# Performance work log

Hardware: AMD Instinct MI355X
Metric: run time of the kernel (lower is better)

The kernel has to match this reference:

```python
import jax, jax.numpy as jnp
import numpy as np

BIG_NEG = -1e9


def setup_inputs() -> dict:
    key = jax.random.key(0)
    ks = jax.random.split(key, 6)
    b, N1, d, C1, K = 4, 511, 64, 31, 32
    features = jax.random.normal(ks[0], (b, N1, d), jnp.float32)
    transition_logits = jax.random.normal(ks[1], (C1, C1), jnp.float32)
    init_logits = jax.random.uniform(ks[2], (C1,), jnp.float32)
    poisson_log_rates = jax.random.normal(ks[3], (C1,), jnp.float32) * 0.5 + 1.5
    A = jax.random.normal(ks[5], (d, d), jnp.float32)
    gaussian_cov = jnp.eye(d, dtype=jnp.float32) + 0.1 * (A @ A.T) / d
    gaussian_means = jax.random.normal(ks[4], (C1, d), jnp.float32) * 0.1
    return {
        "features": features,
        "transition_logits": transition_logits,
        "init_logits": init_logits,
        "poisson_log_rates": poisson_log_rates,
        "gaussian_means": gaussian_means,
        "gaussian_cov": gaussian_cov,
        "max_k": K,
        "add_eos": 1,
    }


def reference(features, transition_logits, init_logits, poisson_log_rates,
              gaussian_means, gaussian_cov, max_k, add_eos):
    b, N1, d = features.shape
    C1 = transition_logits.shape[0]
    K = int(max_k)
    dt = features.dtype

    # transition log-probs: mask diagonal with BIG_NEG, normalize over axis 0 (torch dim=0)
    trans = jax.nn.log_softmax(
        jnp.where(jnp.eye(C1, dtype=bool), jnp.asarray(BIG_NEG, dt), transition_logits), axis=0)
    init = jax.nn.log_softmax(init_logits)

    # Poisson duration log-probs: k*log(rate) - rate - lgamma(k+1), k = 0..K-1
    rates = jnp.exp(poisson_log_rates)  # [C1]
    tsteps = jnp.arange(K, dtype=dt)[:, None]  # [K,1]
    length = tsteps * poisson_log_rates[None, :] - rates[None, :] - jax.scipy.special.gammaln(tsteps + 1.0)  # [K,C1]

    # Gaussian emission log-probs, shared full covariance across classes
    L = jnp.linalg.cholesky(gaussian_cov)
    Linv = jax.scipy.linalg.solve_triangular(L, jnp.eye(d, dtype=dt), lower=True)
    diff = features[:, :, None, :] - gaussian_means[None, None]          # [b,N1,C1,d]
    y = jnp.einsum('bncd,ed->bnce', diff, Linv)
    maha = jnp.sum(y * y, axis=-1)                                       # [b,N1,C1]
    logdet = 2.0 * jnp.sum(jnp.log(jnp.diag(L)))
    emis = -0.5 * (d * jnp.log(jnp.asarray(2.0 * jnp.pi, dt)) + logdet + maha)

    if add_eos:
        N, C = N1 + 1, C1 + 1
        trans_a = jnp.full((C, C), BIG_NEG, dt).at[:C1, :C1].set(trans).at[C1, :].set(0.0)
        init_a = jnp.full((C,), BIG_NEG, dt).at[:C1].set(init)
        length_a = jnp.full((K, C), BIG_NEG, dt).at[:, :C1].set(length).at[1, C1].set(0.0)
        emis_a = jnp.full((b, N, C), BIG_NEG, dt).at[:, :N1, :C1].set(emis).at[:, N1, C1].set(0.0)
    else:
        N, C = N1, C1
        trans_a, init_a, length_a, emis_a = trans, init, length, emis

    ep = jnp.pad(emis_a, ((0, 0), (0, K), (0, 0)))
    cs = jnp.concatenate([jnp.zeros((b, 1, C), dt), jnp.cumsum(ep, axis=1)], axis=1)  # [b,N+K+1,C]
    tt = jnp.arange(N - 1)[:, None]
    kk = jnp.arange(K)[None, :]
    win = cs[:, tt + kk] - cs[:, tt]  # [b, N-1, K, C]

    # edge scores: b x (N-1) x K x C_prev x C
    scores = (trans_a[None, None, None] +
              length_a[None, None, :, None, :] +
              win[:, :, :, None, :])
    scores = scores.at[:, 0].add(init_a[None, None, None, :])
    keos = jnp.arange(1, K)
    scores = scores.at[:, N - 1 - keos, keos].add(emis_a[:, N - 1][:, None, :, None])
    return scores
```

## Files before the change

### kernel.cpp

```cpp
#include <hip/hip_runtime.h>
#include <math.h>

#define BIG_NEG -1.0e9f

typedef float f4 __attribute__((ext_vector_type(4)));

constexpr int B  = 4;
constexpr int N1 = 511;
constexpr int C1 = 31;
constexpr int K  = 32;
constexpr int N  = N1 + 1;
constexpr int C  = C1 + 1;

constexpr int WS_TRANS = 0;
constexpr int WS_INIT  = 1024;
constexpr int WS_LEN   = 1056;
constexpr int WS_P     = 2080;
constexpr int WS_W     = 6176;
constexpr int WS_BIAS  = 8224;
constexpr int WS_EMIS  = 8256;

__global__ __launch_bounds__(512) void k_prep(const float* __restrict__ tl,
                                              const float* __restrict__ il,
                                              const float* __restrict__ plr,
                                              const float* __restrict__ cov,
                                              const float* __restrict__ means,
                                              float* __restrict__ ws) {
    __shared__ float M[64][132];
    __shared__ float cP[2][4][64];
    __shared__ float Bsave[16][16];
    __shared__ float mu[C1][64];

    const int tid = threadIdx.x;
    const int ii = tid >> 3;
    const int cg = tid & 7;

    f4* Mrow = (f4*)&M[ii][0];

    for (int idx = tid; idx < 1024; idx += 512) {
        const int i = idx >> 5, j = idx & 31;
        float lv;
        if (j < C1) {
            float lr = plr[j];
            lv = (float)i * lr - expf(lr) - lgammaf((float)i + 1.0f);
        } else {
            lv = (i == 1) ? 0.0f : BIG_NEG;
        }
        ws[WS_LEN + idx] = lv;
        if (i == C1) ws[WS_TRANS + idx] = 0.0f;
        else if (j == C1) ws[WS_TRANS + idx] = BIG_NEG;
    }
    if (tid < B * C) {
        const int bb = tid >> 5, cc = tid & 31;
        ws[WS_EMIS + (bb * N + N1) * C + cc] = (cc == C1) ? 0.0f : BIG_NEG;
    }
    if (tid < C1) {
        const int jj = tid;
        float m = BIG_NEG;
        for (int r = 0; r < C1; ++r) {
            float v = (r == jj) ? BIG_NEG : tl[r * C1 + jj];
            m = fmaxf(m, v);
        }
        float s = 0.0f;
        for (int r = 0; r < C1; ++r) {
            float v = (r == jj) ? BIG_NEG : tl[r * C1 + jj];
            s += expf(v - m);
        }
        float lse = m + logf(s);
        for (int r = 0; r < C1; ++r) {
            float v = (r == jj) ? BIG_NEG : tl[r * C1 + jj];
            ws[WS_TRANS + r * 32 + jj] = v - lse;
        }
    }
    if (tid == 32) {
        float m = -1.0e30f;
        for (int cc = 0; cc < C1; ++cc) m = fmaxf(m, il[cc]);
        float s = 0.0f;
        for (int cc = 0; cc < C1; ++cc) s += expf(il[cc] - m);
        float lse = m + logf(s);
        for (int cc = 0; cc < C1; ++cc) ws[WS_INIT + cc] = il[cc] - lse;
        ws[WS_INIT + C1] = BIG_NEG;
    }

    {
        Mrow[cg]     = *(const f4*)&cov[ii * 64 + 4 * cg];
        Mrow[cg + 8] = *(const f4*)&cov[ii * 64 + 4 * (cg + 8)];
        const int r0 = 4 * cg, r1 = 4 * (cg + 8);
        f4 e1 = {(ii == r0) ? 1.f : 0.f, (ii == r0 + 1) ? 1.f : 0.f,
                 (ii == r0 + 2) ? 1.f : 0.f, (ii == r0 + 3) ? 1.f : 0.f};
        f4 e2 = {(ii == r1) ? 1.f : 0.f, (ii == r1 + 1) ? 1.f : 0.f,
                 (ii == r1 + 2) ? 1.f : 0.f, (ii == r1 + 3) ? 1.f : 0.f};
        Mrow[cg + 16] = e1;
        Mrow[cg + 24] = e2;
    }
    if (cg == 0) {
        cP[0][0][ii] = cov[ii * 64 + 0];
        cP[0][1][ii] = cov[ii * 64 + 1];
        cP[0][2][ii] = cov[ii * 64 + 2];
        cP[0][3][ii] = cov[ii * 64 + 3];
    }
    for (int idx = tid; idx < C1 * 64; idx += 512)
        mu[idx >> 6][idx & 63] = means[idx];
    __syncthreads();

    float detprod = 1.0f;
    for (int st = 0; st < 16; ++st) {
        const int s = st << 2;
        const int par = st & 1;
        const float T00 = cP[par][0][s + 0], T01 = cP[par][0][s + 1],
                    T02 = cP[par][0][s + 2], T03 = cP[par][0][s + 3];
        const float T10 = cP[par][1][s + 0], T11 = cP[par][1][s + 1],
                    T12 = cP[par][1][s + 2], T13 = cP[par][1][s + 3];
        const float T20 = cP[par][2][s + 0], T21 = cP[par][2][s + 1],
                    T22 = cP[par][2][s + 2], T23 = cP[par][2][s + 3];
        const float T30 = cP[par][3][s + 0], T31 = cP[par][3][s + 1],
                    T32 = cP[par][3][s + 2], T33 = cP[par][3][s + 3];
        const float r0 = __builtin_amdgcn_rcpf(T00);
        const float l10 = T10 * r0, l20 = T20 * r0, l30 = T30 * r0;
        const float u11 = T11 - l10 * T01, u12 = T12 - l10 * T02,
                    u13 = T13 - l10 * T03;
        const float r1 = __builtin_amdgcn_rcpf(u11);
        const float l21 = (T21 - l20 * T01) * r1;
        const float l31 = (T31 - l30 * T01) * r1;
        const float u22 = T22 - l20 * T02 - l21 * u12;
        const float u23 = T23 - l20 * T03 - l21 * u13;
        const float u32 = T32 - l30 * T02 - l31 * u12;
        const float u33t = T33 - l30 * T03 - l31 * u13;
        const float r2 = __builtin_amdgcn_rcpf(u22);
        const float l32 = u32 * r2;
        const float u33 = u33t - l32 * u23;
        const float r3 = __builtin_amdgcn_rcpf(u33);
        detprod *= T00 * u11 * u22 * u33;

        if (tid < 16) Bsave[st][tid] = cP[par][tid & 3][s + (tid >> 2)];

        const float m0 = cP[par][0][ii], m1 = cP[par][1][ii],
                    m2 = cP[par][2][ii], m3 = cP[par][3][ii];
        const float y0 = m0;
        const float y1 = m1 - l10 * y0;
        const float y2 = m2 - l20 * y0 - l21 * y1;
        const float y3 = m3 - l30 * y0 - l31 * y1 - l32 * y2;
        float g3 = y3 * r3;
        float g2 = (y2 - u23 * g3) * r2;
        float g1 = (y1 - u12 * g2 - u13 * g3) * r1;
        float g0 = (y0 - T01 * g1 - T02 * g2 - T03 * g3) * r0;
        const bool pivrow = (unsigned)(ii - s) < 4u;
        if (pivrow) { g0 = 0.f; g1 = 0.f; g2 = 0.f; g3 = 0.f; }

        const f4* Ms0 = (const f4*)&M[s + 0][0];
        const f4* Ms1 = (const f4*)&M[s + 1][0];
        const f4* Ms2 = (const f4*)&M[s + 2][0];
        const f4* Ms3 = (const f4*)&M[s + 3][0];
        const int qpub = st + 1;
#pragma unroll
        for (int h = 0; h < 4; ++h) {
            const int q = cg + 8 * h;
            const int k0 = 4 * q;
            const bool active = (k0 < 64) ? (k0 + 3 >= s) : (k0 - 64 <= s + 3);
            if (!active) continue;
            f4 v = Mrow[q] - g0 * Ms0[q] - g1 * Ms1[q]
                           - g2 * Ms2[q] - g3 * Ms3[q];
            if (!pivrow) Mrow[q] = v;
            if (st < 15 && q == qpub) {
                cP[par ^ 1][0][ii] = v.x;
                cP[par ^ 1][1][ii] = v.y;
                cP[par ^ 1][2][ii] = v.z;
                cP[par ^ 1][3][ii] = v.w;
            }
        }
        __syncthreads();
    }

    {
        const int kb = ii >> 2, rsel = ii & 3, base = kb << 2;
        const float* Bk = &Bsave[kb][0];
        const float T00 = Bk[0],  T01 = Bk[4],  T02 = Bk[8],  T03 = Bk[12];
        const float T10 = Bk[1],  T11 = Bk[5],  T12 = Bk[9],  T13 = Bk[13];
        const float T20 = Bk[2],  T21 = Bk[6],  T22 = Bk[10], T23 = Bk[14];
        const float T30 = Bk[3],  T31 = Bk[7],  T32 = Bk[11], T33 = Bk[15];
        const float r0 = __builtin_amdgcn_rcpf(T00);
        const float l10 = T10 * r0, l20 = T20 * r0, l30 = T30 * r0;
        const float u11 = T11 - l10 * T01, u12 = T12 - l10 * T02,
                    u13 = T13 - l10 * T03;
        const float r1 = __builtin_amdgcn_rcpf(u11);
        const float l21 = (T21 - l20 * T01) * r1;
        const float l31 = (T31 - l30 * T01) * r1;
        const float u22 = T22 - l20 * T02 - l21 * u12;
        const float u23 = T23 - l20 * T03 - l21 * u13;
        const float u32 = T32 - l30 * T02 - l31 * u12;
        const float u33t = T33 - l30 * T03 - l31 * u13;
        const float r2 = __builtin_amdgcn_rcpf(u22);
        const float l32 = u32 * r2;
        const float u33 = u33t - l32 * u23;
        const float r3 = __builtin_amdgcn_rcpf(u33);
        const float m0 = (rsel == 0) ? 1.f : 0.f;
        const float m1 = (rsel == 1) ? 1.f : 0.f;
        const float m2 = (rsel == 2) ? 1.f : 0.f;
        const float m3 = (rsel == 3) ? 1.f : 0.f;
        const float y0 = m0;
        const float y1 = m1 - l10 * y0;
        const float y2 = m2 - l20 * y0 - l21 * y1;
        const float y3 = m3 - l30 * y0 - l31 * y1 - l32 * y2;
        const float x3 = y3 * r3;
        const float x2 = (y2 - u23 * x3) * r2;
        const float x1 = (y1 - u12 * x2 - u13 * x3) * r1;
        const float x0 = (y0 - T01 * x1 - T02 * x2 - T03 * x3) * r0;

        const f4* R0 = (const f4*)&M[base + 0][64];
        const f4* R1 = (const f4*)&M[base + 1][64];
        const f4* R2 = (const f4*)&M[base + 2][64];
        const f4* R3 = (const f4*)&M[base + 3][64];
        f4 va = x0 * R0[cg] + x1 * R1[cg] + x2 * R2[cg] + x3 * R3[cg];
        f4 vb = x0 * R0[cg + 8] + x1 * R1[cg + 8] +
                x2 * R2[cg + 8] + x3 * R3[cg + 8];
        *(f4*)&ws[WS_P + ii * 64 + 4 * cg] = va;
        *(f4*)&ws[WS_P + ii * 64 + 32 + 4 * cg] = vb;
        *(f4*)&M[ii][4 * cg] = va;
        *(f4*)&M[ii][32 + 4 * cg] = vb;
    }
    __syncthreads();

    {
        const int c = tid >> 4;
        const int l = tid & 15;
        if (c < C1) {
            const f4* muc = (const f4*)&mu[c][0];
            float qacc = 0.0f;
#pragma unroll
            for (int h = 0; h < 4; ++h) {
                const int dd = l + 16 * h;
                const f4* Mr = (const f4*)&M[dd][0];
                f4 a4 = {0.f, 0.f, 0.f, 0.f};
#pragma unroll
                for (int e4 = 0; e4 < 16; ++e4) a4 += Mr[e4] * muc[e4];
                float a = (a4.x + a4.y) + (a4.z + a4.w);
                ws[WS_W + dd * 32 + c] = a;
                qacc += a * mu[c][dd];
            }
            for (int m2 = 8; m2 >= 1; m2 >>= 1) qacc += __shfl_xor(qacc, m2, 64);
            if (l == 0)
                ws[WS_BIAS + c] = -0.5f * (64.0f * 1.8378770664093453f +
                                           logf(detprod) + qacc);
        }
    }
}

__global__ __launch_bounds__(256) void k_emis(const float* __restrict__ feat,
                                              float* __restrict__ ws) {
    const int tid = threadIdx.x;
    const int w = tid >> 6, lane = tid & 63;
    const int flat = blockIdx.x * 4 + w;
    const int b = flat / N1, n = flat % N1;
    __shared__ float xs[4][64];

    const float x = feat[flat * 64 + lane];
    xs[w][lane] = x;

    const float* __restrict__ P = ws + WS_P;
    float z = 0.0f;
    for (int dd = 0; dd < 64; ++dd) z += P[dd * 64 + lane] * xs[w][dd];

    float xz = x * z;
    for (int m = 32; m >= 1; m >>= 1) xz += __shfl_xor(xz, m);

    float val = BIG_NEG;
    if (lane < C1) {
        float s = ws[WS_BIAS + lane] - 0.5f * xz;
        const float* __restrict__ wT = ws + WS_W;
        for (int dd = 0; dd < 64; ++dd) s += wT[dd * 32 + lane] * xs[w][dd];
        val = s;
    }
    if (lane < C) ws[WS_EMIS + (b * N + n) * C + lane] = val;
}

__global__ __launch_bounds__(256) void k_main(const float* __restrict__ ws,
                                              float* __restrict__ out) {
    constexpr int TT = 2;
    constexpr int EROWS = TT - 1 + 31;
    const int bid = blockIdx.x;
    const int b = bid >> 8;
    const int t0 = (bid & 255) << 1;
    const int tid = threadIdx.x;

    __shared__ __align__(16) float slen[K * C];
    __shared__ float sh[41][36];

    for (int idx = tid; idx < K * C / 4; idx += 256)
        *(f4*)&slen[4 * idx] = *(const f4*)&ws[WS_LEN + 4 * idx];

    for (int idx = tid; idx < 33 * 8; idx += 256) {
        const int r = idx >> 3, c4 = (idx & 7) << 2;
        const int n = t0 + r;
        f4 v = {0.f, 0.f, 0.f, 0.f};
        if (n < N) v = *(const f4*)&ws[WS_EMIS + (b * N + n) * C + c4];
        *(f4*)&sh[r + 1][c4] = v;
    }
    if (tid < 32) sh[0][tid] = 0.f;
    if (tid >= 64 && tid < 288 - 32) {
        const int z = tid - 64;
        sh[34 + (z >> 5)][z & 31] = 0.f;
    }
    if (tid >= 224 && tid < 256) sh[40][tid - 224] = 0.f;
    __syncthreads();

    {
        const int sc = tid >> 3;
        const int g  = tid & 7;
        float p0 = sh[5 * g + 1][sc];
        float p1 = p0 + sh[5 * g + 2][sc];
        float p2 = p1 + sh[5 * g + 3][sc];
        float p3 = p2 + sh[5 * g + 4][sc];
        float p4 = p3 + sh[5 * g + 5][sc];
        float sum = p4;
#pragma unroll
        for (int off = 1; off < 8; off <<= 1) {
            float nv = __shfl_up(sum, off, 8);
            if (g >= off) sum += nv;
        }
        const float excl = sum - p4;
        sh[5 * g + 1][sc] = p0 + excl;
        sh[5 * g + 2][sc] = p1 + excl;
        sh[5 * g + 3][sc] = p2 + excl;
        sh[5 * g + 4][sc] = p3 + excl;
        sh[5 * g + 5][sc] = p4 + excl;
    }

    const int cp = tid >> 3;
    const int c0 = (tid & 7) << 2;
    const f4 tr4 = *(const f4*)&ws[WS_TRANS + cp * 32 + c0];
    f4 in4 = {0.f, 0.f, 0.f, 0.f};
    if (t0 == 0) in4 = *(const f4*)&ws[WS_INIT + c0];
    const float emisN = (cp == C1) ? 0.0f : BIG_NEG;
    __syncthreads();

#pragma unroll
    for (int j = 0; j < TT; ++j) {
        const int t = t0 + j;
        if (t >= N1) break;
        f4 base_j = tr4;
        if (t == 0) base_j += in4;
        const f4 Sj = *(const f4*)&sh[j][c0];
        const int keos = N1 - t;
        const size_t obase =
            (size_t)(b * N1 + t) * 32768 + (size_t)(cp * 32 + c0);
#pragma unroll 4
        for (int k = 0; k < K; ++k) {
            const f4 len4 = *(const f4*)&slen[k * 32 + c0];
            const f4 win = *(const f4*)&sh[j + k][c0] - Sj;
            f4 o = base_j + len4 + win;
            if (k == keos) o += emisN;
            *(f4*)&out[obase + (size_t)k * 1024] = o;
        }
    }
}

extern "C" void kernel_launch(void* const* d_in, const int* in_sizes, int n_in,
                              void* d_out, int out_size, void* d_ws, size_t ws_size,
                              hipStream_t stream) {
    const float* feat = (const float*)d_in[0];
    const float* tl   = (const float*)d_in[1];
    const float* il   = (const float*)d_in[2];
    const float* plr  = (const float*)d_in[3];
    const float* gm   = (const float*)d_in[4];
    const float* gc   = (const float*)d_in[5];
    float* ws  = (float*)d_ws;
    float* out = (float*)d_out;

    hipLaunchKernelGGL(k_prep, dim3(1), dim3(512), 0, stream, tl, il, plr, gc, gm, ws);
    hipLaunchKernelGGL(k_emis, dim3(B * N1 / 4), dim3(256), 0, stream, feat, ws);
    hipLaunchKernelGGL(k_main, dim3(B * 256), dim3(256), 0, stream, ws, out);
}
```

Measured before the change: 79.57 us.

## Fuse covariance prep into emission kernel by recomputing it per block

New measurement: 83.45 us. +4.9%, slower.

```diff
diff --git a/kernel.cpp b/kernel.cpp
--- a/kernel.cpp
+++ b/kernel.cpp
@@ -15,83 +15,87 @@
 constexpr int WS_TRANS = 0;
 constexpr int WS_INIT  = 1024;
 constexpr int WS_LEN   = 1056;
-constexpr int WS_P     = 2080;
-constexpr int WS_W     = 6176;
-constexpr int WS_BIAS  = 8224;
 constexpr int WS_EMIS  = 8256;
 
-__global__ __launch_bounds__(512) void k_prep(const float* __restrict__ tl,
-                                              const float* __restrict__ il,
-                                              const float* __restrict__ plr,
-                                              const float* __restrict__ cov,
-                                              const float* __restrict__ means,
-                                              float* __restrict__ ws) {
+__global__ __launch_bounds__(256) void k_pe(const float* __restrict__ feat,
+                                            const float* __restrict__ tl,
+                                            const float* __restrict__ il,
+                                            const float* __restrict__ plr,
+                                            const float* __restrict__ cov,
+                                            const float* __restrict__ means,
+                                            float* __restrict__ ws) {
     __shared__ float M[64][132];
     __shared__ float cP[2][4][64];
     __shared__ float Bsave[16][16];
     __shared__ float mu[C1][64];
+    __shared__ float sW[64][32];
+    __shared__ float sb[32];
+    __shared__ float xs[4][64];
 
     const int tid = threadIdx.x;
-    const int ii = tid >> 3;
-    const int cg = tid & 7;
-
+    const int bid = blockIdx.x;
+    const int ii = tid >> 2;
+    const int cg = tid & 3;
     f4* Mrow = (f4*)&M[ii][0];
 
-    for (int idx = tid; idx < 1024; idx += 512) {
-        const int i = idx >> 5, j = idx & 31;
-        float lv;
-        if (j < C1) {
-            float lr = plr[j];
-            lv = (float)i * lr - expf(lr) - lgammaf((float)i + 1.0f);
+    if (bid == 0) {
+        for (int idx = tid; idx < 1024; idx += 256) {
+            const int i = idx >> 5, j = idx & 31;
+            float lv;
+            if (j < C1) {
+                float lr = plr[j];
+                lv = (float)i * lr - expf(lr) - lgammaf((float)i + 1.0f);
+            } else {
+                lv = (i == 1) ? 0.0f : BIG_NEG;
+            }
+            ws[WS_LEN + idx] = lv;
+            if (i == C1) ws[WS_TRANS + idx] = 0.0f;
+            else if (j == C1) ws[WS_TRANS + idx] = BIG_NEG;
+        }
+        if (tid < B * C) {
+            const int bb = tid >> 5, cc = tid & 31;
+            ws[WS_EMIS + (bb * N + N1) * C + cc] = (cc == C1) ? 0.0f : BIG_NEG;
+        }
+        if (tid < C1) {
+            const int jj = tid;
+            float m = BIG_NEG;
+            for (int r = 0; r < C1; ++r) {
+                float v = (r == jj) ? BIG_NEG : tl[r * C1 + jj];
+                m = fmaxf(m, v);
+            }
+            float s = 0.0f;
+            for (int r = 0; r < C1; ++r) {
+                float v = (r == jj) ? BIG_NEG : tl[r * C1 + jj];
+                s += expf(v - m);
+            }
+            float lse = m + logf(s);
+            for (int r = 0; r < C1; ++r) {
+                float v = (r == jj) ? BIG_NEG : tl[r * C1 + jj];
+                ws[WS_TRANS + r * 32 + jj] = v - lse;
+            }
+        }
+        if (tid == 32) {
+            float m = -1.0e30f;
+            for (int cc = 0; cc < C1; ++cc) m = fmaxf(m, il[cc]);
+            float s = 0.0f;
+            for (int cc = 0; cc < C1; ++cc) s += expf(il[cc] - m);
+            float lse = m + logf(s);
+            for (int cc = 0; cc < C1; ++cc) ws[WS_INIT + cc] = il[cc] - lse;
+            ws[WS_INIT + C1] = BIG_NEG;
+        }
+    }
+
+#pragma unroll
+    for (int h = 0; h < 8; ++h) {
+        const int q = cg + 4 * h;
+        if (q < 16) {
+            Mrow[q] = *(const f4*)&cov[ii * 64 + 4 * q];
         } else {
-            lv = (i == 1) ? 0.0f : BIG_NEG;
-        }
-        ws[WS_LEN + idx] = lv;
-        if (i == C1) ws[WS_TRANS + idx] = 0.0f;
-        else if (j == C1) ws[WS_TRANS + idx] = BIG_NEG;
-    }
-    if (tid < B * C) {
-        const int bb = tid >> 5, cc = tid & 31;
-        ws[WS_EMIS + (bb * N + N1) * C + cc] = (cc == C1) ? 0.0f : BIG_NEG;
-    }
-    if (tid < C1) {
-        const int jj = tid;
-        float m = BIG_NEG;
-        for (int r = 0; r < C1; ++r) {
-            float v = (r == jj) ? BIG_NEG : tl[r * C1 + jj];
-            m = fmaxf(m, v);
-        }
-        float s = 0.0f;
-        for (int r = 0; r < C1; ++r) {
-            float v = (r == jj) ? BIG_NEG : tl[r * C1 + jj];
-            s += expf(v - m);
-        }
-        float lse = m + logf(s);
-        for (int r = 0; r < C1; ++r) {
-            float v = (r == jj) ? BIG_NEG : tl[r * C1 + jj];
-            ws[WS_TRANS + r * 32 + jj] = v - lse;
-        }
-    }
-    if (tid == 32) {
-        float m = -1.0e30f;
-        for (int cc = 0; cc < C1; ++cc) m = fmaxf(m, il[cc]);
-        float s = 0.0f;
-        for (int cc = 0; cc < C1; ++cc) s += expf(il[cc] - m);
-        float lse = m + logf(s);
-        for (int cc = 0; cc < C1; ++cc) ws[WS_INIT + cc] = il[cc] - lse;
-        ws[WS_INIT + C1] = BIG_NEG;
-    }
-
-    {
-        Mrow[cg]     = *(const f4*)&cov[ii * 64 + 4 * cg];
-        Mrow[cg + 8] = *(const f4*)&cov[ii * 64 + 4 * (cg + 8)];
-        const int r0 = 4 * cg, r1 = 4 * (cg + 8);
-        f4 e1 = {(ii == r0) ? 1.f : 0.f, (ii == r0 + 1) ? 1.f : 0.f,
-                 (ii == r0 + 2) ? 1.f : 0.f, (ii == r0 + 3) ? 1.f : 0.f};
-        f4 e2 = {(ii == r1) ? 1.f : 0.f, (ii == r1 + 1) ? 1.f : 0.f,
-                 (ii == r1 + 2) ? 1.f : 0.f, (ii == r1 + 3) ? 1.f : 0.f};
-        Mrow[cg + 16] = e1;
-        Mrow[cg + 24] = e2;
+            const int r0 = 4 * (q - 16);
+            f4 e = {(ii == r0) ? 1.f : 0.f, (ii == r0 + 1) ? 1.f : 0.f,
+                    (ii == r0 + 2) ? 1.f : 0.f, (ii == r0 + 3) ? 1.f : 0.f};
+            Mrow[q] = e;
+        }
     }
     if (cg == 0) {
         cP[0][0][ii] = cov[ii * 64 + 0];
@@ -99,7 +103,7 @@
         cP[0][2][ii] = cov[ii * 64 + 2];
         cP[0][3][ii] = cov[ii * 64 + 3];
     }
-    for (int idx = tid; idx < C1 * 64; idx += 512)
+    for (int idx = tid; idx < C1 * 64; idx += 256)
         mu[idx >> 6][idx & 63] = means[idx];
     __syncthreads();
 
@@ -153,8 +157,8 @@
         const f4* Ms3 = (const f4*)&M[s + 3][0];
         const int qpub = st + 1;
 #pragma unroll
-        for (int h = 0; h < 4; ++h) {
-            const int q = cg + 8 * h;
+        for (int h = 0; h < 8; ++h) {
+            const int q = cg + 4 * h;
             const int k0 = 4 * q;
             const bool active = (k0 < 64) ? (k0 + 3 >= s) : (k0 - 64 <= s + 3);
             if (!active) continue;
@@ -210,73 +214,67 @@
         const f4* R1 = (const f4*)&M[base + 1][64];
         const f4* R2 = (const f4*)&M[base + 2][64];
         const f4* R3 = (const f4*)&M[base + 3][64];
-        f4 va = x0 * R0[cg] + x1 * R1[cg] + x2 * R2[cg] + x3 * R3[cg];
-        f4 vb = x0 * R0[cg + 8] + x1 * R1[cg + 8] +
-                x2 * R2[cg + 8] + x3 * R3[cg + 8];
-        *(f4*)&ws[WS_P + ii * 64 + 4 * cg] = va;
-        *(f4*)&ws[WS_P + ii * 64 + 32 + 4 * cg] = vb;
-        *(f4*)&M[ii][4 * cg] = va;
-        *(f4*)&M[ii][32 + 4 * cg] = vb;
+#pragma unroll
+        for (int h = 0; h < 4; ++h) {
+            const int j = cg + 4 * h;
+            f4 v = x0 * R0[j] + x1 * R1[j] + x2 * R2[j] + x3 * R3[j];
+            *(f4*)&M[ii][4 * j] = v;
+        }
     }
     __syncthreads();
 
     {
-        const int c = tid >> 4;
-        const int l = tid & 15;
+        const int c = tid >> 3;
+        const int l = tid & 7;
         if (c < C1) {
             const f4* muc = (const f4*)&mu[c][0];
             float qacc = 0.0f;
 #pragma unroll
-            for (int h = 0; h < 4; ++h) {
-                const int dd = l + 16 * h;
+            for (int h = 0; h < 8; ++h) {
+                const int dd = l + 8 * h;
                 const f4* Mr = (const f4*)&M[dd][0];
                 f4 a4 = {0.f, 0.f, 0.f, 0.f};
 #pragma unroll
                 for (int e4 = 0; e4 < 16; ++e4) a4 += Mr[e4] * muc[e4];
                 float a = (a4.x + a4.y) + (a4.z + a4.w);
-                ws[WS_W + dd * 32 + c] = a;
+                sW[dd][c] = a;
                 qacc += a * mu[c][dd];
             }
-            for (int m2 = 8; m2 >= 1; m2 >>= 1) qacc += __shfl_xor(qacc, m2, 64);
+            for (int m2 = 4; m2 >= 1; m2 >>= 1)
+                qacc += __shfl_xor(qacc, m2, 8);
             if (l == 0)
-                ws[WS_BIAS + c] = -0.5f * (64.0f * 1.8378770664093453f +
-                                           logf(detprod) + qacc);
-        }
-    }
-}
-
-__global__ __launch_bounds__(256) void k_emis(const float* __restrict__ feat,
-                                              float* __restrict__ ws) {
-    const int tid = threadIdx.x;
-    const int w = tid >> 6, lane = tid & 63;
-    const int flat = blockIdx.x * 4 + w;
-    const int b = flat / N1, n = flat % N1;
-    __shared__ float xs[4][64];
-
-    const float x = feat[flat * 64 + lane];
-    xs[w][lane] = x;
-
-    const float* __restrict__ P = ws + WS_P;
-    float z = 0.0f;
-    for (int dd = 0; dd < 64; ++dd) z += P[dd * 64 + lane] * xs[w][dd];
-
-    float xz = x * z;
-    for (int m = 32; m >= 1; m >>= 1) xz += __shfl_xor(xz, m);
-
-    float val = BIG_NEG;
-    if (lane < C1) {
-        float s = ws[WS_BIAS + lane] - 0.5f * xz;
-        const float* __restrict__ wT = ws + WS_W;
-        for (int dd = 0; dd < 64; ++dd) s += wT[dd * 32 + lane] * xs[w][dd];
-        val = s;
-    }
-    if (lane < C) ws[WS_EMIS + (b * N + n) * C + lane] = val;
+                sb[c] = -0.5f * (64.0f * 1.8378770664093453f +
+                                 logf(detprod) + qacc);
+        }
+    }
+    __syncthreads();
+
+    {
+        const int w = tid >> 6, lane = tid & 63;
+        const int flat = bid * 4 + w;
+        const int b = flat / N1, n = flat - b * N1;
+        const float x = feat[flat * 64 + lane];
+        xs[w][lane] = x;
+
+        float z = 0.0f;
+        for (int dd = 0; dd < 64; ++dd) z += M[dd][lane] * xs[w][dd];
+
+        float xz = x * z;
+        for (int m2 = 32; m2 >= 1; m2 >>= 1) xz += __shfl_xor(xz, m2);
+
+        float val = BIG_NEG;
+        if (lane < C1) {
+            float s = sb[lane] - 0.5f * xz;
+            for (int dd = 0; dd < 64; ++dd) s += sW[dd][lane] * xs[w][dd];
+            val = s;
+        }
+        if (lane < C) ws[WS_EMIS + (b * N + n) * C + lane] = val;
+    }
 }
 
 __global__ __launch_bounds__(256) void k_main(const float* __restrict__ ws,
                                               float* __restrict__ out) {
     constexpr int TT = 2;
-    constexpr int EROWS = TT - 1 + 31;
     const int bid = blockIdx.x;
     const int b = bid >> 8;
     const int t0 = (bid & 255) << 1;
@@ -366,7 +364,7 @@
     float* ws  = (float*)d_ws;
     float* out = (float*)d_out;
 
-    hipLaunchKernelGGL(k_prep, dim3(1), dim3(512), 0, stream, tl, il, plr, gc, gm, ws);
-    hipLaunchKernelGGL(k_emis, dim3(B * N1 / 4), dim3(256), 0, stream, feat, ws);
+    hipLaunchKernelGGL(k_pe, dim3(B * N1 / 4), dim3(256), 0, stream,
+                       feat, tl, il, plr, gc, gm, ws);
     hipLaunchKernelGGL(k_main, dim3(B * 256), dim3(256), 0, stream, ws, out);
 }
```
